# Kernel tuning notes

Measured on AMD Instinct MI355X. Metric: run time of the kernel, lower is better.

Reference implementation:

```python
import jax, jax.numpy as jnp
import numpy as np

NUM_NODES = 100000
NUM_EDGES = 1200000
IN_CH = 64
HID_CH = 64
NUM_REL = 8
DEG = NUM_EDGES // NUM_NODES  # uniform degree 12


def setup_inputs() -> dict:
    key = jax.random.key(0)
    k1, k2, k3, k4 = jax.random.split(key, 4)
    x = jax.random.normal(k1, (NUM_NODES, IN_CH), dtype=jnp.float32)
    linear = jax.random.normal(k2, (NUM_REL, IN_CH, HID_CH), dtype=jnp.float32) * (1.0 / np.sqrt(IN_CH))
    ptr = jnp.arange(NUM_NODES + 1, dtype=jnp.int64) * DEG  # CSR row pointers, uniform degree
    idx = jax.random.randint(k3, (NUM_EDGES,), 0, NUM_NODES, dtype=jnp.int64)
    edge_types = jax.random.randint(k4, (NUM_EDGES,), 0, NUM_REL, dtype=jnp.int64)
    return {"x": x, "linear": linear, "ptr": ptr, "idx": idx,
            "edge_types": edge_types, "num_node": NUM_NODES}


def reference(x, linear, ptr, idx, edge_types, num_node):
    # Gather source-node features per edge: [E, in]
    gathered = x[idx]
    # Per-edge-type linear transform (loop over small fixed num_rel, like RGCNOP)
    out_e = jnp.zeros((gathered.shape[0], linear.shape[-1]), dtype=gathered.dtype)
    for r in range(linear.shape[0]):
        mask = (edge_types == r).astype(gathered.dtype)[:, None]
        out_e = out_e + mask * (gathered @ linear[r])
    # CSR scatter-sum aggregation over destination segments defined by ptr
    num_edges = idx.shape[0]
    seg_ids = jnp.searchsorted(ptr, jnp.arange(num_edges, dtype=ptr.dtype), side='right') - 1
    agg = jax.ops.segment_sum(out_e, seg_ids, num_segments=num_node)
    # Degree normalization
    deg = (ptr[1:] - ptr[:-1]).astype(agg.dtype)
    return agg / deg[:, None]
```

## Files before the change

### kernel.cpp

```cpp
#include <hip/hip_runtime.h>
#include <hip/hip_bf16.h>


#define THREADS 512
#define NPB 64
#define KDIM 512
#define LDA 520
#define MAXE 1024
#define WFRAG (4 * 16 * 64 * 8)

typedef __attribute__((ext_vector_type(8))) short bf16x8;
typedef __attribute__((ext_vector_type(4))) float f32x4;

extern __shared__ __align__(16) char smem[];

__device__ __forceinline__ unsigned short f2bf(float f) {
  __hip_bfloat16 h = __float2bfloat16(f);
  return *reinterpret_cast<unsigned short*>(&h);
}

__global__ __launch_bounds__(256) void pack_w(const void* __restrict__ wv,
                                              unsigned short* __restrict__ wsB) {
  const int lane = threadIdx.x & 63;
  const unsigned word = ((const unsigned*)wv)[lane];
  const int exf = (int)((word >> 7) & 0xFFu);
  const bool w_bf16 = __popcll(__ballot(exf >= 96 && exf < 160)) >= 48;
  for (int i = blockIdx.x * 256 + threadIdx.x; i < WFRAG; i += gridDim.x * 256) {
    const int j  = i & 7;
    const int l  = (i >> 3) & 63;
    const int kt = (i >> 9) & 15;
    const int nt = i >> 13;
    const int k  = kt * 32 + (l >> 4) * 8 + j;
    const int n  = nt * 16 + (l & 15);
    float v;
    if (w_bf16) v = __bfloat162float(((const __hip_bfloat16*)wv)[k * 64 + n]);
    else        v = ((const float*)wv)[k * 64 + n];
    wsB[i] = f2bf(v);
  }
}

#define ACC_SW(accrow, r, vv)                                        \
  switch (r) {                                                       \
    case 0: accrow[0] += (vv); break; case 1: accrow[1] += (vv); break; \
    case 2: accrow[2] += (vv); break; case 3: accrow[3] += (vv); break; \
    case 4: accrow[4] += (vv); break; case 5: accrow[5] += (vv); break; \
    case 6: accrow[6] += (vv); break; default: accrow[7] += (vv); break; }

__global__ __launch_bounds__(THREADS, 2)
void rgcn_fused(const void* __restrict__ xv,
                const void* __restrict__ wv,
                const int* __restrict__ p32,
                const int* __restrict__ i32,
                const int* __restrict__ t32,
                const unsigned short* __restrict__ wsB,
                float* __restrict__ out,
                int num_nodes) {
  __hip_bfloat16* aggS = (__hip_bfloat16*)smem;
  __hip_bfloat16* wtS  = aggS + NPB * LDA;
  char* tail = smem + (size_t)NPB * LDA * 2 + (wsB ? 0 : (size_t)64 * LDA * 2);
  float*    invS  = (float*)tail;
  int*      ptrS  = (int*)(tail + 256);
  unsigned* eMeta = (unsigned*)(tail + 256 + 272);

  const int tid   = threadIdx.x;
  const int lane  = tid & 63;
  const int wvid  = tid >> 6;
  const int node0 = blockIdx.x * NPB;

  const unsigned xword = ((const unsigned*)xv)[lane];
  const int exf = (int)((xword >> 7) & 0xFFu);
  const bool x_bf16 = __popcll(__ballot(exf >= 96 && exf < 160)) >= 48;
  const bool idx64 = (p32[1] == 0);

  auto ldptr = [&](int n) -> int { return idx64 ? p32[2 * n] : p32[n]; };

  const int ntop   = min(node0 + NPB, num_nodes);
  const int e_lo   = ldptr(node0);
  const int ecount = ldptr(ntop) - e_lo;
  const bool staged = (ecount > 0 && ecount <= MAXE);

  for (int i = tid; i <= NPB; i += THREADS)
    ptrS[i] = ldptr(min(node0 + i, num_nodes));

  if (staged) {
    for (int e = tid; e < ecount; e += THREADS) {
      const int ge = e_lo + e;
      const unsigned s = (unsigned)(idx64 ? i32[2 * ge] : i32[ge]);
      const unsigned r = (unsigned)(idx64 ? t32[2 * ge] : t32[ge]);
      eMeta[e] = s | (r << 24);
    }
  }

  if (!wsB) {
    if (x_bf16) {
      const __hip_bfloat16* wb = (const __hip_bfloat16*)wv;
      for (int i = tid; i < KDIM * 64; i += THREADS)
        wtS[(i & 63) * LDA + (i >> 6)] = wb[i];
    } else {
      const float* wf = (const float*)wv;
      for (int i = tid; i < KDIM * 64; i += THREADS)
        wtS[(i & 63) * LDA + (i >> 6)] = __float2bfloat16(wf[i]);
    }
  }

  __syncthreads();

  for (int i = tid; i < NPB; i += THREADS) {
    const int d = ptrS[i + 1] - ptrS[i];
    invS[i] = (d > 0 && node0 + i < num_nodes) ? 1.0f / (float)d : 0.0f;
  }

  const int c16 = lane & 15;
  const int qd  = lane >> 4;

  auto gather = [&](auto xp, auto loadrow) {
#pragma unroll
    for (int g = 0; g < 2; ++g) {
      const int nlb = wvid * 8 + g * 4;
      const int eq0 = ptrS[nlb + qd] - e_lo;
      const int dq  = ptrS[nlb + qd + 1] - e_lo - eq0;
      const bool okfast = staged && (node0 + nlb + 3 < num_nodes) &&
                          (__ballot(dq == 12) == ~0ull);
      if (okfast) {
        unsigned m[12];
#pragma unroll
        for (int j = 0; j < 12; ++j) m[j] = eMeta[eq0 + j];
        float4 v[12];
#pragma unroll
        for (int j = 0; j < 12; ++j)
          v[j] = loadrow((int)(m[j] & 0x00FFFFFFu), c16);
        float4 acc[8];
#pragma unroll
        for (int r = 0; r < 8; ++r) acc[r] = make_float4(0.f, 0.f, 0.f, 0.f);
#pragma unroll
        for (int j = 0; j < 12; ++j) {
          const unsigned rj = m[j] >> 24;
#pragma unroll
          for (int r = 0; r < 8; ++r) {
            const float mk = (rj == (unsigned)r) ? 1.0f : 0.0f;
            acc[r].x += mk * v[j].x;
            acc[r].y += mk * v[j].y;
            acc[r].z += mk * v[j].z;
            acc[r].w += mk * v[j].w;
          }
        }
        unsigned short* dst = (unsigned short*)(aggS + (nlb + qd) * LDA) + 4 * c16;
#pragma unroll
        for (int r = 0; r < 8; ++r) {
          ushort4 b;
          b.x = f2bf(acc[r].x); b.y = f2bf(acc[r].y);
          b.z = f2bf(acc[r].z); b.w = f2bf(acc[r].w);
          *(ushort4*)(dst + r * 64) = b;
        }
      } else {
#pragma unroll
        for (int t = 0; t < 4; ++t) {
          const int nl = nlb + t;
          float a[8] = {0.f, 0.f, 0.f, 0.f, 0.f, 0.f, 0.f, 0.f};
          if (node0 + nl < num_nodes) {
            const int e0 = ptrS[nl] - e_lo, e1 = ptrS[nl + 1] - e_lo;
            for (int e = e0; e < e1; ++e) {
              unsigned mm;
              if (staged) mm = eMeta[e];
              else {
                const int ge = e_lo + e;
                mm = (unsigned)(idx64 ? i32[2 * ge] : i32[ge]) |
                     ((unsigned)(idx64 ? t32[2 * ge] : t32[ge]) << 24);
              }
              const float vv = (float)xp[(size_t)(mm & 0x00FFFFFFu) * 64 + lane];
              const int r = __builtin_amdgcn_readfirstlane((int)(mm >> 24));
              ACC_SW(a, r, vv)
            }
          }
#pragma unroll
          for (int r = 0; r < 8; ++r)
            aggS[nl * LDA + r * 64 + lane] = __float2bfloat16(a[r]);
        }
      }
    }
  };

  if (x_bf16) {
    const __hip_bfloat16* xb = (const __hip_bfloat16*)xv;
    auto lr = [&](int src, int c) -> float4 {
      const ushort4 u = ((const ushort4*)xv)[src * 16 + c];
      float4 f;
      f.x = __uint_as_float((unsigned)(unsigned short)u.x << 16);
      f.y = __uint_as_float((unsigned)(unsigned short)u.y << 16);
      f.z = __uint_as_float((unsigned)(unsigned short)u.z << 16);
      f.w = __uint_as_float((unsigned)(unsigned short)u.w << 16);
      return f;
    };
    gather(xb, lr);
  } else {
    const float* xf = (const float*)xv;
    auto lr = [&](int src, int c) -> float4 {
      return ((const float4*)xv)[src * 16 + c];
    };
    gather(xf, lr);
  }

  __syncthreads();

  const int mt  = wvid >> 1;
  const int nt0 = (wvid & 1) * 2;
  const int mi  = lane & 15;
  const int q4  = lane >> 4;
  const __hip_bfloat16* ap = aggS + (mt * 16 + mi) * LDA + q4 * 8;
  f32x4 c0 = {0.f, 0.f, 0.f, 0.f};
  f32x4 c1 = {0.f, 0.f, 0.f, 0.f};
  if (wsB) {
    const bf16x8* B = (const bf16x8*)wsB;
#pragma unroll
    for (int kt = 0; kt < KDIM / 32; ++kt) {
      const bf16x8 a  = *(const bf16x8*)(ap + kt * 32);
      const bf16x8 b0 = B[((nt0 + 0) * 16 + kt) * 64 + lane];
      const bf16x8 b1 = B[((nt0 + 1) * 16 + kt) * 64 + lane];
      c0 = __builtin_amdgcn_mfma_f32_16x16x32_bf16(a, b0, c0, 0, 0, 0);
      c1 = __builtin_amdgcn_mfma_f32_16x16x32_bf16(a, b1, c1, 0, 0, 0);
    }
  } else {
    const __hip_bfloat16* bp0 = wtS + ((nt0 + 0) * 16 + mi) * LDA + q4 * 8;
    const __hip_bfloat16* bp1 = wtS + ((nt0 + 1) * 16 + mi) * LDA + q4 * 8;
#pragma unroll
    for (int kt = 0; kt < KDIM / 32; ++kt) {
      const bf16x8 a  = *(const bf16x8*)(ap  + kt * 32);
      const bf16x8 b0 = *(const bf16x8*)(bp0 + kt * 32);
      const bf16x8 b1 = *(const bf16x8*)(bp1 + kt * 32);
      c0 = __builtin_amdgcn_mfma_f32_16x16x32_bf16(a, b0, c0, 0, 0, 0);
      c1 = __builtin_amdgcn_mfma_f32_16x16x32_bf16(a, b1, c1, 0, 0, 0);
    }
  }

#pragma unroll
  for (int i = 0; i < 4; ++i) {
    const int row  = q4 * 4 + i;
    const int nl   = mt * 16 + row;
    const int node = node0 + nl;
    if (node < num_nodes) {
      const float s = invS[nl];
      out[(size_t)node * 64 + (nt0 + 0) * 16 + mi] = c0[i] * s;
      out[(size_t)node * 64 + (nt0 + 1) * 16 + mi] = c1[i] * s;
    }
  }
}

extern "C" void kernel_launch(void* const* d_in, const int* in_sizes, int n_in,
                              void* d_out, int out_size, void* d_ws, size_t ws_size,
                              hipStream_t stream) {
  const void* x   = d_in[0];
  const void* w   = d_in[1];
  const int*  ptr = (const int*)d_in[2];
  const int*  idx = (const int*)d_in[3];
  const int*  et  = (const int*)d_in[4];
  float*      out = (float*)d_out;

  const int num_nodes = in_sizes[0] / 64;

  const bool useWs = (d_ws != nullptr) &&
                     (ws_size >= (size_t)WFRAG * sizeof(unsigned short));
  unsigned short* wsB = useWs ? (unsigned short*)d_ws : nullptr;
  if (useWs) pack_w<<<32, 256, 0, stream>>>(w, wsB);

  const size_t lds_bytes = (size_t)NPB * LDA * 2 +
                           (useWs ? 0 : (size_t)64 * LDA * 2) +
                           256 + 272 + (size_t)MAXE * 4;

  hipFuncSetAttribute((const void*)rgcn_fused,
                      hipFuncAttributeMaxDynamicSharedMemorySize,
                      (int)lds_bytes);

  const int nblocks = (num_nodes + NPB - 1) / NPB;
  rgcn_fused<<<nblocks, THREADS, lds_bytes, stream>>>(x, w, ptr, idx, et, wsB,
                                                      out, num_nodes);
}
```

Baseline: 138.4 us.

## Halve nodes per block and gather one row per wave with scalar metadata

Halves the nodes handled per block to 32 and raises the launch-bounds occupancy hint from 2 to 8 blocks per CU, which means more, smaller blocks and less LDS per block. The gather fast path changes from four nodes per wave with float4 loads and masked accumulation over all relation types to one node per wave. Each lane loads one scalar feature, edge metadata is made wave-uniform with readfirstlane, and accumulation uses a switch on the relation type. The MFMA stage now gives each wave a single 16x16 output tile. The aim is more latency hiding through higher occupancy, at the cost of narrower memory loads and fewer independent loads in flight per lane.

```diff
diff --git a/kernel.cpp b/kernel.cpp
--- a/kernel.cpp
+++ b/kernel.cpp
@@ -3,10 +3,10 @@
 
 
 #define THREADS 512
-#define NPB 64
+#define NPB 32
 #define KDIM 512
 #define LDA 520
-#define MAXE 1024
+#define MAXE 512
 #define WFRAG (4 * 16 * 64 * 8)
 
 typedef __attribute__((ext_vector_type(8))) short bf16x8;
@@ -46,7 +46,7 @@
     case 4: accrow[4] += (vv); break; case 5: accrow[5] += (vv); break; \
     case 6: accrow[6] += (vv); break; default: accrow[7] += (vv); break; }
 
-__global__ __launch_bounds__(THREADS, 2)
+__global__ __launch_bounds__(THREADS, 8)
 void rgcn_fused(const void* __restrict__ xv,
                 const void* __restrict__ wv,
                 const int* __restrict__ p32,
@@ -60,7 +60,7 @@
   char* tail = smem + (size_t)NPB * LDA * 2 + (wsB ? 0 : (size_t)64 * LDA * 2);
   float*    invS  = (float*)tail;
   int*      ptrS  = (int*)(tail + 256);
-  unsigned* eMeta = (unsigned*)(tail + 256 + 272);
+  unsigned* eMeta = (unsigned*)(tail + 256 + 144);
 
   const int tid   = threadIdx.x;
   const int lane  = tid & 63;
@@ -110,125 +110,92 @@
     invS[i] = (d > 0 && node0 + i < num_nodes) ? 1.0f / (float)d : 0.0f;
   }
 
-  const int c16 = lane & 15;
-  const int qd  = lane >> 4;
-
-  auto gather = [&](auto xp, auto loadrow) {
-#pragma unroll
-    for (int g = 0; g < 2; ++g) {
-      const int nlb = wvid * 8 + g * 4;
-      const int eq0 = ptrS[nlb + qd] - e_lo;
-      const int dq  = ptrS[nlb + qd + 1] - e_lo - eq0;
-      const bool okfast = staged && (node0 + nlb + 3 < num_nodes) &&
-                          (__ballot(dq == 12) == ~0ull);
-      if (okfast) {
-        unsigned m[12];
-#pragma unroll
-        for (int j = 0; j < 12; ++j) m[j] = eMeta[eq0 + j];
-        float4 v[12];
+  auto gather = [&](auto lc) {
+    for (int t = 0; t < 4; ++t) {
+      const int nl  = wvid * 4 + t;
+      const int pe0 = __builtin_amdgcn_readfirstlane(ptrS[nl]);
+      const int pe1 = __builtin_amdgcn_readfirstlane(ptrS[nl + 1]);
+      const int e0  = pe0 - e_lo;
+      const int dg  = pe1 - pe0;
+      const bool inb = (node0 + nl < num_nodes);
+      if (staged && inb && dg == 12) {
+        int m[12];
 #pragma unroll
         for (int j = 0; j < 12; ++j)
-          v[j] = loadrow((int)(m[j] & 0x00FFFFFFu), c16);
-        float4 acc[8];
-#pragma unroll
-        for (int r = 0; r < 8; ++r) acc[r] = make_float4(0.f, 0.f, 0.f, 0.f);
+          m[j] = __builtin_amdgcn_readfirstlane((int)eMeta[e0 + j]);
+        float v[12];
+#pragma unroll
+        for (int j = 0; j < 12; ++j)
+          v[j] = lc((int)((unsigned)m[j] & 0x00FFFFFFu));
+        float acc[8] = {0.f, 0.f, 0.f, 0.f, 0.f, 0.f, 0.f, 0.f};
 #pragma unroll
         for (int j = 0; j < 12; ++j) {
-          const unsigned rj = m[j] >> 24;
-#pragma unroll
-          for (int r = 0; r < 8; ++r) {
-            const float mk = (rj == (unsigned)r) ? 1.0f : 0.0f;
-            acc[r].x += mk * v[j].x;
-            acc[r].y += mk * v[j].y;
-            acc[r].z += mk * v[j].z;
-            acc[r].w += mk * v[j].w;
+          const int r = (int)((unsigned)m[j] >> 24);
+          ACC_SW(acc, r, v[j])
+        }
+#pragma unroll
+        for (int r = 0; r < 8; ++r)
+          aggS[nl * LDA + r * 64 + lane] = __float2bfloat16(acc[r]);
+      } else {
+        float a[8] = {0.f, 0.f, 0.f, 0.f, 0.f, 0.f, 0.f, 0.f};
+        if (inb) {
+          const int ee0 = pe0 - e_lo, ee1 = pe1 - e_lo;
+          for (int e = ee0; e < ee1; ++e) {
+            unsigned mm;
+            if (staged) mm = eMeta[e];
+            else {
+              const int ge = e_lo + e;
+              mm = (unsigned)(idx64 ? i32[2 * ge] : i32[ge]) |
+                   ((unsigned)(idx64 ? t32[2 * ge] : t32[ge]) << 24);
+            }
+            const float vv = lc((int)(mm & 0x00FFFFFFu));
+            const int r = __builtin_amdgcn_readfirstlane((int)(mm >> 24));
+            ACC_SW(a, r, vv)
           }
         }
-        unsigned short* dst = (unsigned short*)(aggS + (nlb + qd) * LDA) + 4 * c16;
-#pragma unroll
-        for (int r = 0; r < 8; ++r) {
-          ushort4 b;
-          b.x = f2bf(acc[r].x); b.y = f2bf(acc[r].y);
-          b.z = f2bf(acc[r].z); b.w = f2bf(acc[r].w);
-          *(ushort4*)(dst + r * 64) = b;
-        }
-      } else {
-#pragma unroll
-        for (int t = 0; t < 4; ++t) {
-          const int nl = nlb + t;
-          float a[8] = {0.f, 0.f, 0.f, 0.f, 0.f, 0.f, 0.f, 0.f};
-          if (node0 + nl < num_nodes) {
-            const int e0 = ptrS[nl] - e_lo, e1 = ptrS[nl + 1] - e_lo;
-            for (int e = e0; e < e1; ++e) {
-              unsigned mm;
-              if (staged) mm = eMeta[e];
-              else {
-                const int ge = e_lo + e;
-                mm = (unsigned)(idx64 ? i32[2 * ge] : i32[ge]) |
-                     ((unsigned)(idx64 ? t32[2 * ge] : t32[ge]) << 24);
-              }
-              const float vv = (float)xp[(size_t)(mm & 0x00FFFFFFu) * 64 + lane];
-              const int r = __builtin_amdgcn_readfirstlane((int)(mm >> 24));
-              ACC_SW(a, r, vv)
-            }
-          }
-#pragma unroll
-          for (int r = 0; r < 8; ++r)
-            aggS[nl * LDA + r * 64 + lane] = __float2bfloat16(a[r]);
-        }
+#pragma unroll
+        for (int r = 0; r < 8; ++r)
+          aggS[nl * LDA + r * 64 + lane] = __float2bfloat16(a[r]);
       }
     }
   };
 
   if (x_bf16) {
-    const __hip_bfloat16* xb = (const __hip_bfloat16*)xv;
-    auto lr = [&](int src, int c) -> float4 {
-      const ushort4 u = ((const ushort4*)xv)[src * 16 + c];
-      float4 f;
-      f.x = __uint_as_float((unsigned)(unsigned short)u.x << 16);
-      f.y = __uint_as_float((unsigned)(unsigned short)u.y << 16);
-      f.z = __uint_as_float((unsigned)(unsigned short)u.z << 16);
-      f.w = __uint_as_float((unsigned)(unsigned short)u.w << 16);
-      return f;
+    auto lc = [&](int s) -> float {
+      const unsigned short u = ((const unsigned short*)xv)[((size_t)s << 6) + lane];
+      return __uint_as_float((unsigned)u << 16);
     };
-    gather(xb, lr);
+    gather(lc);
   } else {
-    const float* xf = (const float*)xv;
-    auto lr = [&](int src, int c) -> float4 {
-      return ((const float4*)xv)[src * 16 + c];
+    auto lc = [&](int s) -> float {
+      return ((const float*)xv)[((size_t)s << 6) + lane];
     };
-    gather(xf, lr);
+    gather(lc);
   }
 
   __syncthreads();
 
-  const int mt  = wvid >> 1;
-  const int nt0 = (wvid & 1) * 2;
-  const int mi  = lane & 15;
-  const int q4  = lane >> 4;
+  const int mt = wvid >> 2;
+  const int nt = wvid & 3;
+  const int mi = lane & 15;
+  const int q4 = lane >> 4;
   const __hip_bfloat16* ap = aggS + (mt * 16 + mi) * LDA + q4 * 8;
   f32x4 c0 = {0.f, 0.f, 0.f, 0.f};
-  f32x4 c1 = {0.f, 0.f, 0.f, 0.f};
   if (wsB) {
     const bf16x8* B = (const bf16x8*)wsB;
 #pragma unroll
     for (int kt = 0; kt < KDIM / 32; ++kt) {
-      const bf16x8 a  = *(const bf16x8*)(ap + kt * 32);
-      const bf16x8 b0 = B[((nt0 + 0) * 16 + kt) * 64 + lane];
-      const bf16x8 b1 = B[((nt0 + 1) * 16 + kt) * 64 + lane];
-      c0 = __builtin_amdgcn_mfma_f32_16x16x32_bf16(a, b0, c0, 0, 0, 0);
-      c1 = __builtin_amdgcn_mfma_f32_16x16x32_bf16(a, b1, c1, 0, 0, 0);
+      const bf16x8 a = *(const bf16x8*)(ap + kt * 32);
+      const bf16x8 b = B[(nt * 16 + kt) * 64 + lane];
+      c0 = __builtin_amdgcn_mfma_f32_16x16x32_bf16(a, b, c0, 0, 0, 0);
     }
   } else {
-    const __hip_bfloat16* bp0 = wtS + ((nt0 + 0) * 16 + mi) * LDA + q4 * 8;
-    const __hip_bfloat16* bp1 = wtS + ((nt0 + 1) * 16 + mi) * LDA + q4 * 8;
+    const __hip_bfloat16* bp = wtS + (nt * 16 + mi) * LDA + q4 * 8;
 #pragma unroll
     for (int kt = 0; kt < KDIM / 32; ++kt) {
-      const bf16x8 a  = *(const bf16x8*)(ap  + kt * 32);
-      const bf16x8 b0 = *(const bf16x8*)(bp0 + kt * 32);
-      const bf16x8 b1 = *(const bf16x8*)(bp1 + kt * 32);
-      c0 = __builtin_amdgcn_mfma_f32_16x16x32_bf16(a, b0, c0, 0, 0, 0);
-      c1 = __builtin_amdgcn_mfma_f32_16x16x32_bf16(a, b1, c1, 0, 0, 0);
+      const bf16x8 a = *(const bf16x8*)(ap + kt * 32);
+      const bf16x8 b = *(const bf16x8*)(bp + kt * 32);
+      c0 = __builtin_amdgcn_mfma_f32_16x16x32_bf16(a, b, c0, 0, 0, 0);
     }
   }
 
@@ -238,9 +205,7 @@
     const int nl   = mt * 16 + row;
     const int node = node0 + nl;
     if (node < num_nodes) {
-      const float s = invS[nl];
-      out[(size_t)node * 64 + (nt0 + 0) * 16 + mi] = c0[i] * s;
-      out[(size_t)node * 64 + (nt0 + 1) * 16 + mi] = c1[i] * s;
+      out[(size_t)node * 64 + nt * 16 + mi] = c0[i] * invS[nl];
     }
   }
 }
@@ -264,7 +229,7 @@
 
   const size_t lds_bytes = (size_t)NPB * LDA * 2 +
                            (useWs ? 0 : (size_t)64 * LDA * 2) +
-                           256 + 272 + (size_t)MAXE * 4;
+                           256 + 144 + (size_t)MAXE * 4;
 
   hipFuncSetAttribute((const void*)rgcn_fused,
                       hipFuncAttributeMaxDynamicSharedMemorySize,
```

Measured after the change: 145.3 us. 5.0% more time.
